# Performance work log

Measured on AMD Instinct MI355X. Metric: run time of the kernel, lower is better.

## Reference

```python
import jax, jax.numpy as jnp
import numpy as np

B, S, DIM = 2, 2048, 512
NH, QK, VD = 8, 128, 128
NEG = -1e9


def setup_inputs() -> dict:
    key = jax.random.key(0)
    ks = jax.random.split(key, 10)
    scale = 0.02
    x = jax.random.normal(ks[0], (B, S, DIM), dtype=jnp.float32)
    pos_embedding = jax.random.normal(ks[1], (NH, S, S), dtype=jnp.float32) * scale
    # causal additive mask: 0 on/below diagonal, large negative above
    mask = jnp.where(jnp.tril(jnp.ones((S, S), dtype=bool)), 0.0, NEG).astype(jnp.float32)
    wq_w = jax.random.normal(ks[2], (DIM, NH * QK), dtype=jnp.float32) * scale
    wq_b = jax.random.normal(ks[3], (NH * QK,), dtype=jnp.float32) * scale
    wk_w = jax.random.normal(ks[4], (DIM, NH * QK), dtype=jnp.float32) * scale
    wk_b = jax.random.normal(ks[5], (NH * QK,), dtype=jnp.float32) * scale
    wv_w = jax.random.normal(ks[6], (DIM, NH * VD), dtype=jnp.float32) * scale
    wv_b = jax.random.normal(ks[7], (NH * VD,), dtype=jnp.float32) * scale
    wo_w = jax.random.normal(ks[8], (NH * VD, DIM), dtype=jnp.float32) * scale
    wo_b = jax.random.normal(ks[9], (DIM,), dtype=jnp.float32) * scale
    return {
        "x": x, "start_pos": 0, "mask": mask, "pos_embedding": pos_embedding,
        "wq_w": wq_w, "wq_b": wq_b, "wk_w": wk_w, "wk_b": wk_b,
        "wv_w": wv_w, "wv_b": wv_b, "wo_w": wo_w, "wo_b": wo_b,
    }


def reference(x, start_pos, mask, pos_embedding,
              wq_w, wq_b, wk_w, wk_b, wv_w, wv_b, wo_w, wo_b):
    b, s, _ = x.shape
    # per-head positional bias slice [NH, s, s]
    pe = pos_embedding[:, start_pos:start_pos + s, start_pos:start_pos + s]
    q = (x @ wq_w + wq_b).reshape(b, s, NH, QK)
    k = (x @ wk_w + wk_b).reshape(b, s, NH, QK)
    v = (x @ wv_w + wv_b).reshape(b, s, NH, VD)
    # unfused attention: full [b, h, s, S] score tensor
    score = jnp.einsum('bshk,bShk->bhsS', q, k) / np.float32(np.sqrt(QK))
    score = score + pe[None] + mask[None, None, :s, :s]
    score = jax.nn.softmax(score, axis=-1).astype(x.dtype)
    out = jnp.einsum('bhsS,bShv->bshv', score, v).reshape(b, s, NH * VD)
    return out @ wo_w + wo_b
```

## Files before the change

kernel.cpp:

```cpp
#include <hip/hip_runtime.h>
#include <hip/hip_bf16.h>
#include <stdint.h>

#define BB_ 2
#define SS_ 2048
#define DIM_ 512
#define NH_ 8
#define QK_ 128
#define VD_ 128

typedef __attribute__((ext_vector_type(8))) short bf16x8;
typedef __attribute__((ext_vector_type(4))) float f32x4;
typedef __attribute__((ext_vector_type(8))) unsigned short ushort8;
typedef __attribute__((ext_vector_type(4))) unsigned short ushort4v;

__device__ __forceinline__ unsigned short f2bf(float f) {
  union { float f; unsigned int u; } v; v.f = f;
  unsigned int r = v.u + 0x7FFFu + ((v.u >> 16) & 1u);
  return (unsigned short)(r >> 16);
}

__device__ __forceinline__ float bf2f(unsigned short u) {
  union { unsigned int u; float f; } v; v.u = ((unsigned int)u) << 16;
  return v.f;
}

__device__ __forceinline__ f32x4 mfma16(bf16x8 a, bf16x8 b, f32x4 c) {
  return __builtin_amdgcn_mfma_f32_16x16x32_bf16(a, b, c, 0, 0, 0);
}


__global__ void k_convert_x(const float* __restrict__ x, unsigned short* __restrict__ xb, int n4) {
  int i = blockIdx.x * blockDim.x + threadIdx.x;
  if (i < n4) {
    float4 v = reinterpret_cast<const float4*>(x)[i];
    ushort4v o;
    o[0] = f2bf(v.x); o[1] = f2bf(v.y); o[2] = f2bf(v.z); o[3] = f2bf(v.w);
    reinterpret_cast<ushort4v*>(xb)[i] = o;
  }
}

__global__ void k_transpose_cvt(const float* __restrict__ src, unsigned short* __restrict__ dst,
                                int R, int C) {
  __shared__ float t[64][65];
  const int c0 = blockIdx.x * 64, r0 = blockIdx.y * 64;
  const int tid = threadIdx.x;
  const int rr = tid >> 4, cc4 = (tid & 15) * 4;
#pragma unroll
  for (int p = 0; p < 4; p++) {
    float4 v = *reinterpret_cast<const float4*>(src + (size_t)(r0 + rr + p * 16) * C + c0 + cc4);
    t[rr + p * 16][cc4 + 0] = v.x; t[rr + p * 16][cc4 + 1] = v.y;
    t[rr + p * 16][cc4 + 2] = v.z; t[rr + p * 16][cc4 + 3] = v.w;
  }
  __syncthreads();
  const int cl = tid >> 2, rb = (tid & 3) * 16;
#pragma unroll
  for (int g = 0; g < 2; g++) {
    ushort8 o;
#pragma unroll
    for (int j = 0; j < 8; j++) o[j] = f2bf(t[rb + g * 8 + j][cl]);
    *reinterpret_cast<ushort8*>(dst + (size_t)(c0 + cl) * R + r0 + rb + g * 8) = o;
  }
}

__global__ void k_concat_bias(const float* __restrict__ bq, const float* __restrict__ bk,
                              const float* __restrict__ bv, float* __restrict__ out) {
  int i = blockIdx.x * blockDim.x + threadIdx.x;
  if (i < 1024) out[i] = bq[i];
  else if (i < 2048) out[i] = bk[i - 1024];
  else if (i < 3072) out[i] = bv[i - 2048];
}


template <int EPI>
__global__ __launch_bounds__(256) void k_gemm_bt(
    const unsigned short* __restrict__ A, const unsigned short* __restrict__ BT,
    const float* __restrict__ bias, int K,
    unsigned short* __restrict__ oq, unsigned short* __restrict__ ok,
    unsigned short* __restrict__ ovt, float* __restrict__ of) {
  __shared__ __align__(16) unsigned short Al[128][32];
  __shared__ __align__(16) unsigned short Bl[128][32];
  const int tid = threadIdx.x;
  const int lane = tid & 63, wave = tid >> 6;
  const int wm = wave >> 1, wn = wave & 1;
  const int lr = lane & 15, lg = lane >> 4;
  const int m0 = blockIdx.y * 128, n0 = blockIdx.x * 128;
  f32x4 acc[4][4] = {};
  const int srow = lane >> 2, scol = (lane & 3) * 8;

  for (int k0 = 0; k0 < K; k0 += 32) {
    __syncthreads();
    {
      const unsigned short* ga = A + (size_t)(m0 + wave * 16 + srow) * K + k0 + scol;
      __builtin_amdgcn_global_load_lds((const unsigned int*)ga,
                                       (unsigned int*)&Al[wave * 16][0], 16, 0, 0);
      __builtin_amdgcn_global_load_lds((const unsigned int*)(ga + (size_t)64 * K),
                                       (unsigned int*)&Al[wave * 16 + 64][0], 16, 0, 0);
      const unsigned short* gb = BT + (size_t)(n0 + wave * 16 + srow) * K + k0 + scol;
      __builtin_amdgcn_global_load_lds((const unsigned int*)gb,
                                       (unsigned int*)&Bl[wave * 16][0], 16, 0, 0);
      __builtin_amdgcn_global_load_lds((const unsigned int*)(gb + (size_t)64 * K),
                                       (unsigned int*)&Bl[wave * 16 + 64][0], 16, 0, 0);
    }
    __syncthreads();
    bf16x8 af[4], bfr[4];
#pragma unroll
    for (int i = 0; i < 4; i++)
      af[i] = *reinterpret_cast<const bf16x8*>(&Al[wm * 64 + i * 16 + lr][lg * 8]);
#pragma unroll
    for (int i = 0; i < 4; i++)
      bfr[i] = *reinterpret_cast<const bf16x8*>(&Bl[wn * 64 + i * 16 + lr][lg * 8]);
#pragma unroll
    for (int i = 0; i < 4; i++)
#pragma unroll
      for (int j = 0; j < 4; j++)
        acc[i][j] = mfma16(af[i], bfr[j], acc[i][j]);
  }

#pragma unroll
  for (int i = 0; i < 4; i++) {
#pragma unroll
    for (int j = 0; j < 4; j++) {
      const int n = n0 + wn * 64 + j * 16 + lr;
      const float bv = bias[n];
      const int mb = m0 + wm * 64 + i * 16 + lg * 4;
      if (EPI == 0) {
        const int region = n >> 10;
        const int h = (n & 1023) >> 7, d = n & 127;
        const int bb = mb >> 11, s0 = mb & 2047;
        const size_t hb = (size_t)(bb * NH_ + h) << 18;
        if (region == 2) {
          ushort4v pk;
#pragma unroll
          for (int r = 0; r < 4; r++) pk[r] = f2bf(acc[i][j][r] + bv);
          const int s32 = s0 >> 5, sg = (s0 >> 3) & 3, e0 = s0 & 7;
          const size_t off = hb + (size_t)(((s32 * 8 + (d >> 4)) * 4 + sg) * 128 + (d & 15) * 8 + e0);
          *reinterpret_cast<ushort4v*>(ovt + off) = pk;
        } else {
          unsigned short* dst = ((region == 0) ? oq : ok) + hb;
          const float qs = (region == 0) ? 0.08838834764831845f : 1.0f;
          const int rt_ = s0 >> 4, c_ = d >> 5, lg_ = (d >> 3) & 3, e_ = d & 7;
          const int lrb = s0 & 15;
#pragma unroll
          for (int r = 0; r < 4; r++)
            dst[(size_t)(((rt_ * 4 + c_) * 64 + lg_ * 16 + lrb + r) * 8 + e_)] =
                f2bf((acc[i][j][r] + bv) * qs);
        }
      } else {
#pragma unroll
        for (int r = 0; r < 4; r++) {
          const int m = mb + r;
          of[(size_t)m * DIM_ + n] = acc[i][j][r] + bv;
        }
      }
    }
  }
}


__global__ __launch_bounds__(256, 2) void k_attn(
    const unsigned short* __restrict__ q, const unsigned short* __restrict__ k,
    const unsigned short* __restrict__ vt, const float* __restrict__ pe,
    unsigned short* __restrict__ att) {
  __shared__ __align__(16) unsigned short P[4][2][16][72];
  __shared__ __align__(16) unsigned short Xo[4][32][136];
  __shared__ float Xml[4][32][2];

  const int h = blockIdx.x, p = blockIdx.y, b = blockIdx.z;
  const int lane = threadIdx.x & 63, wave = threadIdx.x >> 6;
  const int lr = lane & 15, lg = lane >> 4;

  const size_t hb = (size_t)(b * NH_ + h) << 18;
  const unsigned short* qfp = q + hb;
  const unsigned short* kfp = k + hb;
  const unsigned short* vfp = vt + hb;
  const float* peh = pe + (size_t)h * SS_ * SS_;

  for (int phase = 0; phase < 2; phase++) {
    const int rt = phase ? (63 - p) : p;
    const int myq0 = rt * 32 + lr;
    const float* pep = peh + (size_t)myq0 * SS_;

    bf16x8 qf[2][4];
#pragma unroll
    for (int t = 0; t < 2; t++)
#pragma unroll
      for (int c = 0; c < 4; c++)
        qf[t][c] = *reinterpret_cast<const bf16x8*>(
            qfp + ((size_t)((rt * 2 + t) * 4 + c) << 9) + (lane << 3));

    f32x4 o[2][8] = {};
    float m[2] = {-1e30f, -1e30f}, l[2] = {0.f, 0.f};

    const int nkt = (rt >> 1) + 1;
    const int kt_lo = (nkt * wave) >> 2;
    const int kt_hi = (nkt * (wave + 1)) >> 2;

    for (int kt = kt_lo; kt < kt_hi; kt++) {
      const int kbase = kt * 64;

      bf16x8 vf[8];
#pragma unroll
      for (int sub = 0; sub < 8; sub++)
        vf[sub] = *reinterpret_cast<const bf16x8*>(
            vfp + ((size_t)((kt * 2) * 8 + sub) << 9) + (lane << 3));

      f32x4 sc[2][4];
#pragma unroll
      for (int t = 0; t < 2; t++)
#pragma unroll
        for (int ck = 0; ck < 4; ck++)
          sc[t][ck] = *reinterpret_cast<const f32x4*>(
              pep + (size_t)(t * 16) * SS_ + kbase + ck * 16 + lg * 4);

      __builtin_amdgcn_s_setprio(1);
#pragma unroll
      for (int ck = 0; ck < 4; ck++) {
#pragma unroll
        for (int c = 0; c < 4; c++) {
          const bf16x8 kf = *reinterpret_cast<const bf16x8*>(
              kfp + ((size_t)((kt * 4 + ck) * 4 + c) << 9) + (lane << 3));
          sc[0][ck] = mfma16(kf, qf[0][c], sc[0][ck]);
          sc[1][ck] = mfma16(kf, qf[1][c], sc[1][ck]);
        }
      }
      __builtin_amdgcn_s_setprio(0);

      const bool diag = (kt == nkt - 1);
      float ps[2], rsum[2];
#pragma unroll
      for (int t = 0; t < 2; t++) {
        const int mq = myq0 + t * 16;
        float tm = -1e30f;
#pragma unroll
        for (int ck = 0; ck < 4; ck++) {
#pragma unroll
          for (int r = 0; r < 4; r++) {
            float v = sc[t][ck][r];
            if (diag && (kbase + ck * 16 + lg * 4 + r) > mq) v = -1e30f;
            sc[t][ck][r] = v;
            tm = fmaxf(tm, v);
          }
        }
        tm = fmaxf(tm, __shfl_xor(tm, 16));
        tm = fmaxf(tm, __shfl_xor(tm, 32));
        const float mnew = fmaxf(m[t], tm);
        ps[t] = __expf(m[t] - mnew);
        m[t] = mnew;
        float rs = 0.f;
#pragma unroll
        for (int ck = 0; ck < 4; ck++)
#pragma unroll
          for (int r = 0; r < 4; r++) {
            const float pv = __expf(sc[t][ck][r] - mnew);
            sc[t][ck][r] = pv;
            rs += pv;
          }
        rsum[t] = rs;
      }
#pragma unroll
      for (int t = 0; t < 2; t++) {
        float rs = rsum[t];
        rs += __shfl_xor(rs, 16);
        rs += __shfl_xor(rs, 32);
        l[t] = l[t] * ps[t] + rs;
#pragma unroll
        for (int sub = 0; sub < 8; sub++)
#pragma unroll
          for (int r = 0; r < 4; r++) o[t][sub][r] *= ps[t];
#pragma unroll
        for (int ck = 0; ck < 4; ck++) {
          ushort4v pk;
#pragma unroll
          for (int r = 0; r < 4; r++) pk[r] = f2bf(sc[t][ck][r]);
          *reinterpret_cast<ushort4v*>(&P[wave][t][lr][ck * 16 + lg * 4]) = pk;
        }
      }

      __builtin_amdgcn_s_setprio(1);
#pragma unroll
      for (int t = 0; t < 2; t++) {
        const bf16x8 pf = *reinterpret_cast<const bf16x8*>(&P[wave][t][lr][lg * 8]);
#pragma unroll
        for (int sub = 0; sub < 8; sub++)
          o[t][sub] = mfma16(vf[sub], pf, o[t][sub]);
      }
      __builtin_amdgcn_s_setprio(0);
#pragma unroll
      for (int sub = 0; sub < 8; sub++)
        vf[sub] = *reinterpret_cast<const bf16x8*>(
            vfp + ((size_t)((kt * 2 + 1) * 8 + sub) << 9) + (lane << 3));
      __builtin_amdgcn_s_setprio(1);
#pragma unroll
      for (int t = 0; t < 2; t++) {
        const bf16x8 pf = *reinterpret_cast<const bf16x8*>(&P[wave][t][lr][32 + lg * 8]);
#pragma unroll
        for (int sub = 0; sub < 8; sub++)
          o[t][sub] = mfma16(vf[sub], pf, o[t][sub]);
      }
      __builtin_amdgcn_s_setprio(0);
    }

#pragma unroll
    for (int t = 0; t < 2; t++) {
      const float inv = (l[t] > 0.f) ? 1.0f / l[t] : 0.f;
#pragma unroll
      for (int sub = 0; sub < 8; sub++) {
        ushort4v pk;
#pragma unroll
        for (int r = 0; r < 4; r++) pk[r] = f2bf(o[t][sub][r] * inv);
        *reinterpret_cast<ushort4v*>(&Xo[wave][t * 16 + lr][sub * 16 + lg * 4]) = pk;
      }
      if (lg == 0) { Xml[wave][t * 16 + lr][0] = m[t]; Xml[wave][t * 16 + lr][1] = l[t]; }
    }
    __syncthreads();

    {
      const int mrow = wave * 8 + (lane >> 3);
      float mm[4], ll[4];
      float ms = -1e30f;
#pragma unroll
      for (int w = 0; w < 4; w++) {
        mm[w] = Xml[w][mrow][0]; ll[w] = Xml[w][mrow][1];
        ms = fmaxf(ms, mm[w]);
      }
      float c[4], csum = 0.f;
#pragma unroll
      for (int w = 0; w < 4; w++) { c[w] = __expf(mm[w] - ms) * ll[w]; csum += c[w]; }
      const float invT = 1.0f / csum;
#pragma unroll
      for (int half = 0; half < 2; half++) {
        const int dc = (lane & 7) + half * 8;
        float acc[8] = {};
#pragma unroll
        for (int w = 0; w < 4; w++) {
          const ushort8 v = *reinterpret_cast<const ushort8*>(&Xo[w][mrow][dc * 8]);
#pragma unroll
          for (int e = 0; e < 8; e++) acc[e] += c[w] * bf2f(v[e]);
        }
        ushort8 outv;
#pragma unroll
        for (int e = 0; e < 8; e++) outv[e] = f2bf(acc[e] * invT);
        *reinterpret_cast<ushort8*>(
            att + (size_t)(b * SS_ + rt * 32 + mrow) * (NH_ * VD_) + h * VD_ + dc * 8) = outv;
      }
    }
    __syncthreads();
  }
}


extern "C" void kernel_launch(void* const* d_in, const int* in_sizes, int n_in,
                              void* d_out, int out_size, void* d_ws, size_t ws_size,
                              hipStream_t stream) {
  const float* x    = (const float*)d_in[0];
  const float* pe   = (const float*)d_in[3];
  const float* wq_w = (const float*)d_in[4];
  const float* wq_b = (const float*)d_in[5];
  const float* wk_w = (const float*)d_in[6];
  const float* wk_b = (const float*)d_in[7];
  const float* wv_w = (const float*)d_in[8];
  const float* wv_b = (const float*)d_in[9];
  const float* wo_w = (const float*)d_in[10];
  const float* wo_b = (const float*)d_in[11];
  float* out = (float*)d_out;

  char* ws = (char*)d_ws;
  unsigned short* x_bf   = (unsigned short*)(ws);
  unsigned short* wqkv_t = (unsigned short*)(ws + 4194304);
  unsigned short* wo_t   = (unsigned short*)(ws + 7340032);
  float*          qkv_b  = (float*)(ws + 8388608);
  unsigned short* qb     = (unsigned short*)(ws + 8400896);
  unsigned short* kb     = (unsigned short*)(ws + 16789504);
  unsigned short* vtb    = (unsigned short*)(ws + 25178112);
  unsigned short* attb   = (unsigned short*)(ws + 33566720);

  k_convert_x<<<2048, 256, 0, stream>>>(x, x_bf, (4096 * 512) / 4);
  {
    dim3 gt(16, 8);
    k_transpose_cvt<<<gt, 256, 0, stream>>>(wq_w, wqkv_t, 512, 1024);
    k_transpose_cvt<<<gt, 256, 0, stream>>>(wk_w, wqkv_t + 1024 * 512, 512, 1024);
    k_transpose_cvt<<<gt, 256, 0, stream>>>(wv_w, wqkv_t + 2048 * 512, 512, 1024);
    dim3 gt2(8, 16);
    k_transpose_cvt<<<gt2, 256, 0, stream>>>(wo_w, wo_t, 1024, 512);
  }
  k_concat_bias<<<12, 256, 0, stream>>>(wq_b, wk_b, wv_b, qkv_b);

  dim3 g1(24, 32);
  k_gemm_bt<0><<<g1, 256, 0, stream>>>(x_bf, wqkv_t, qkv_b, 512, qb, kb, vtb, nullptr);

  dim3 g2(NH_, 32, BB_);
  k_attn<<<g2, 256, 0, stream>>>(qb, kb, vtb, pe, attb);

  dim3 g3(4, 32);
  k_gemm_bt<1><<<g3, 256, 0, stream>>>(attb, wo_t, wo_b, 1024, nullptr, nullptr, nullptr, out);
}
```

Baseline: 119.3 us.

## Merge prep kernels, prefetch positional bias, and skip rescale when max stable

Folds the x conversion, the four weight transposes and the bias concat into one launch to cut kernel-launch overhead. In attention, the positional-bias tile for the next key block is loaded one iteration early so its latency overlaps the score MFMAs. It also adds a lazy-rescale rule: when every lane's new row max is within 8 of the running max, the max is kept and the exp and O rescale are skipped, which lets exponent values grow up to e^8 and adds register pressure from the prefetch buffer.

```diff
diff --git a/kernel.cpp b/kernel.cpp
--- a/kernel.cpp
+++ b/kernel.cpp
@@ -30,45 +30,55 @@
 }
 
 
-__global__ void k_convert_x(const float* __restrict__ x, unsigned short* __restrict__ xb, int n4) {
-  int i = blockIdx.x * blockDim.x + threadIdx.x;
-  if (i < n4) {
+__device__ void transpose_tile(const float* __restrict__ src, unsigned short* __restrict__ dst,
+                               int R, int C, int c0, int r0, int tid, float (*t)[65]) {
+  const int rr = tid >> 4, cc4 = (tid & 15) * 4;
+#pragma unroll
+  for (int p = 0; p < 4; p++) {
+    float4 v = *reinterpret_cast<const float4*>(src + (size_t)(r0 + rr + p * 16) * C + c0 + cc4);
+    t[rr + p * 16][cc4 + 0] = v.x; t[rr + p * 16][cc4 + 1] = v.y;
+    t[rr + p * 16][cc4 + 2] = v.z; t[rr + p * 16][cc4 + 3] = v.w;
+  }
+  __syncthreads();
+  const int cl = tid >> 2, rb = (tid & 3) * 16;
+#pragma unroll
+  for (int g = 0; g < 2; g++) {
+    ushort8 o;
+#pragma unroll
+    for (int j = 0; j < 8; j++) o[j] = f2bf(t[rb + g * 8 + j][cl]);
+    *reinterpret_cast<ushort8*>(dst + (size_t)(c0 + cl) * R + r0 + rb + g * 8) = o;
+  }
+}
+
+__global__ void k_prep(const float* __restrict__ x, unsigned short* __restrict__ xb,
+                       const float* __restrict__ wq, const float* __restrict__ wk,
+                       const float* __restrict__ wv, unsigned short* __restrict__ wqkv_t,
+                       const float* __restrict__ wo, unsigned short* __restrict__ wo_t,
+                       const float* __restrict__ bq, const float* __restrict__ bk,
+                       const float* __restrict__ bv, float* __restrict__ bias_out) {
+  __shared__ float t[64][65];
+  const int bid = blockIdx.x, tid = threadIdx.x;
+  if (bid < 2048) {
+    const int i = bid * 256 + tid;
     float4 v = reinterpret_cast<const float4*>(x)[i];
     ushort4v o;
     o[0] = f2bf(v.x); o[1] = f2bf(v.y); o[2] = f2bf(v.z); o[3] = f2bf(v.w);
     reinterpret_cast<ushort4v*>(xb)[i] = o;
-  }
-}
-
-__global__ void k_transpose_cvt(const float* __restrict__ src, unsigned short* __restrict__ dst,
-                                int R, int C) {
-  __shared__ float t[64][65];
-  const int c0 = blockIdx.x * 64, r0 = blockIdx.y * 64;
-  const int tid = threadIdx.x;
-  const int rr = tid >> 4, cc4 = (tid & 15) * 4;
-#pragma unroll
-  for (int p = 0; p < 4; p++) {
-    float4 v = *reinterpret_cast<const float4*>(src + (size_t)(r0 + rr + p * 16) * C + c0 + cc4);
-    t[rr + p * 16][cc4 + 0] = v.x; t[rr + p * 16][cc4 + 1] = v.y;
-    t[rr + p * 16][cc4 + 2] = v.z; t[rr + p * 16][cc4 + 3] = v.w;
-  }
-  __syncthreads();
-  const int cl = tid >> 2, rb = (tid & 3) * 16;
-#pragma unroll
-  for (int g = 0; g < 2; g++) {
-    ushort8 o;
-#pragma unroll
-    for (int j = 0; j < 8; j++) o[j] = f2bf(t[rb + g * 8 + j][cl]);
-    *reinterpret_cast<ushort8*>(dst + (size_t)(c0 + cl) * R + r0 + rb + g * 8) = o;
-  }
-}
-
-__global__ void k_concat_bias(const float* __restrict__ bq, const float* __restrict__ bk,
-                              const float* __restrict__ bv, float* __restrict__ out) {
-  int i = blockIdx.x * blockDim.x + threadIdx.x;
-  if (i < 1024) out[i] = bq[i];
-  else if (i < 2048) out[i] = bk[i - 1024];
-  else if (i < 3072) out[i] = bv[i - 2048];
+  } else if (bid < 2432) {
+    const int tt0 = bid - 2048;
+    const int w = tt0 >> 7, tt = tt0 & 127;
+    const float* src = (w == 0) ? wq : (w == 1) ? wk : wv;
+    transpose_tile(src, wqkv_t + (size_t)w * 1024 * 512, 512, 1024,
+                   (tt & 15) * 64, (tt >> 4) * 64, tid, t);
+  } else if (bid < 2560) {
+    const int tt = bid - 2432;
+    transpose_tile(wo, wo_t, 1024, 512, (tt & 7) * 64, (tt >> 3) * 64, tid, t);
+  } else {
+    const int i = (bid - 2560) * 256 + tid;
+    if (i < 1024) bias_out[i] = bq[i];
+    else if (i < 2048) bias_out[i] = bk[i - 1024];
+    else if (i < 3072) bias_out[i] = bv[i - 2048];
+  }
 }
 
 
@@ -196,22 +206,40 @@
     const int kt_lo = (nkt * wave) >> 2;
     const int kt_hi = (nkt * (wave + 1)) >> 2;
 
+    f32x4 pe_pre[2][4];
+    if (kt_lo < kt_hi) {
+#pragma unroll
+      for (int t = 0; t < 2; t++)
+#pragma unroll
+        for (int ck = 0; ck < 4; ck++)
+          pe_pre[t][ck] = *reinterpret_cast<const f32x4*>(
+              pep + (size_t)(t * 16) * SS_ + kt_lo * 64 + ck * 16 + lg * 4);
+    }
+
     for (int kt = kt_lo; kt < kt_hi; kt++) {
       const int kbase = kt * 64;
+
+      f32x4 sc[2][4];
+#pragma unroll
+      for (int t = 0; t < 2; t++)
+#pragma unroll
+        for (int ck = 0; ck < 4; ck++)
+          sc[t][ck] = pe_pre[t][ck];
+
+      if (kt + 1 < kt_hi) {
+#pragma unroll
+        for (int t = 0; t < 2; t++)
+#pragma unroll
+          for (int ck = 0; ck < 4; ck++)
+            pe_pre[t][ck] = *reinterpret_cast<const f32x4*>(
+                pep + (size_t)(t * 16) * SS_ + (kt + 1) * 64 + ck * 16 + lg * 4);
+      }
 
       bf16x8 vf[8];
 #pragma unroll
       for (int sub = 0; sub < 8; sub++)
         vf[sub] = *reinterpret_cast<const bf16x8*>(
             vfp + ((size_t)((kt * 2) * 8 + sub) << 9) + (lane << 3));
-
-      f32x4 sc[2][4];
-#pragma unroll
-      for (int t = 0; t < 2; t++)
-#pragma unroll
-        for (int ck = 0; ck < 4; ck++)
-          sc[t][ck] = *reinterpret_cast<const f32x4*>(
-              pep + (size_t)(t * 16) * SS_ + kbase + ck * 16 + lg * 4);
 
       __builtin_amdgcn_s_setprio(1);
 #pragma unroll
@@ -228,6 +256,7 @@
 
       const bool diag = (kt == nkt - 1);
       float ps[2], rsum[2];
+      bool df[2];
 #pragma unroll
       for (int t = 0; t < 2; t++) {
         const int mq = myq0 + t * 16;
@@ -244,15 +273,20 @@
         }
         tm = fmaxf(tm, __shfl_xor(tm, 16));
         tm = fmaxf(tm, __shfl_xor(tm, 32));
-        const float mnew = fmaxf(m[t], tm);
-        ps[t] = __expf(m[t] - mnew);
-        m[t] = mnew;
+        df[t] = (__all(tm <= m[t] + 8.0f) != 0);
+        if (df[t]) {
+          ps[t] = 1.0f;
+        } else {
+          const float mnew = fmaxf(m[t], tm);
+          ps[t] = __expf(m[t] - mnew);
+          m[t] = mnew;
+        }
         float rs = 0.f;
 #pragma unroll
         for (int ck = 0; ck < 4; ck++)
 #pragma unroll
           for (int r = 0; r < 4; r++) {
-            const float pv = __expf(sc[t][ck][r] - mnew);
+            const float pv = __expf(sc[t][ck][r] - m[t]);
             sc[t][ck][r] = pv;
             rs += pv;
           }
@@ -264,10 +298,12 @@
         rs += __shfl_xor(rs, 16);
         rs += __shfl_xor(rs, 32);
         l[t] = l[t] * ps[t] + rs;
-#pragma unroll
-        for (int sub = 0; sub < 8; sub++)
-#pragma unroll
-          for (int r = 0; r < 4; r++) o[t][sub][r] *= ps[t];
+        if (!df[t]) {
+#pragma unroll
+          for (int sub = 0; sub < 8; sub++)
+#pragma unroll
+            for (int r = 0; r < 4; r++) o[t][sub][r] *= ps[t];
+        }
 #pragma unroll
         for (int ck = 0; ck < 4; ck++) {
           ushort4v pk;
@@ -375,16 +411,8 @@
   unsigned short* vtb    = (unsigned short*)(ws + 25178112);
   unsigned short* attb   = (unsigned short*)(ws + 33566720);
 
-  k_convert_x<<<2048, 256, 0, stream>>>(x, x_bf, (4096 * 512) / 4);
-  {
-    dim3 gt(16, 8);
-    k_transpose_cvt<<<gt, 256, 0, stream>>>(wq_w, wqkv_t, 512, 1024);
-    k_transpose_cvt<<<gt, 256, 0, stream>>>(wk_w, wqkv_t + 1024 * 512, 512, 1024);
-    k_transpose_cvt<<<gt, 256, 0, stream>>>(wv_w, wqkv_t + 2048 * 512, 512, 1024);
-    dim3 gt2(8, 16);
-    k_transpose_cvt<<<gt2, 256, 0, stream>>>(wo_w, wo_t, 1024, 512);
-  }
-  k_concat_bias<<<12, 256, 0, stream>>>(wq_b, wk_b, wv_b, qkv_b);
+  k_prep<<<2572, 256, 0, stream>>>(x, x_bf, wq_w, wk_w, wv_w, wqkv_t,
+                                   wo_w, wo_t, wq_b, wk_b, wv_b, qkv_b);
 
   dim3 g1(24, 32);
   k_gemm_bt<0><<<g1, 256, 0, stream>>>(x_bf, wqkv_t, qkv_b, 512, qb, kb, vtb, nullptr);
```

After: 131.2 us. +10.0%, slower.
